# Kernel tuning notes

Measured on AMD Instinct MI355X. Metric: run time of the kernel, lower is better.

## Reference

```python
import jax, jax.numpy as jnp
import numpy as np

B, LQ, LK, D = 8, 1024, 4096, 1024


def setup_inputs() -> dict:
    key = jax.random.key(0)
    k1, k2, k3, k4, k5, k6 = jax.random.split(key, 6)
    s = 1.0 / np.sqrt(D)
    return {
        "T": jax.random.normal(k1, (B, LQ, D), dtype=jnp.float32),
        "S": jax.random.normal(k2, (B, LK, D), dtype=jnp.float32),
        "Wq": jax.random.uniform(k3, (D, D), jnp.float32, -s, s),
        "Wk": jax.random.uniform(k4, (D, D), jnp.float32, -s, s),
        "Wv": jax.random.uniform(k5, (D, D), jnp.float32, -s, s),
        "Wo": jax.random.uniform(k6, (D, D), jnp.float32, -s, s),
    }


def reference(T, S, Wq, Wk, Wv, Wo):
    # Linear layers: y = x @ W.T (torch nn.Linear convention), bias=False
    q = jnp.einsum('bqd,ed->bqe', T, Wq)          # [B, LQ, D]
    k = jnp.einsum('bkd,ed->bke', S, Wk)          # [B, LK, D]
    v = jnp.einsum('bkd,ed->bke', S, Wv)          # [B, LK, D]
    scale = jnp.asarray(D, q.dtype) ** -0.5        # hidden_dim ** -0.5 (single head)
    attn = jnp.einsum('bqe,bke->bqk', q, k) * scale  # [B, LQ, LK]
    attn = jax.nn.softmax(attn, axis=-1)
    out = jnp.einsum('bqk,bke->bqe', attn, v)      # [B, LQ, D]
    return jnp.einsum('bqe,fe->bqf', out, Wo)      # output projection
```

## Files before the change

kernel.cpp:

```cpp
#include <hip/hip_runtime.h>
#include <stdint.h>

typedef __bf16 bf16;
typedef __bf16 bf16x8 __attribute__((ext_vector_type(8)));
typedef float f32x4 __attribute__((ext_vector_type(4)));

__device__ __forceinline__ void gload_lds16(const void* g, void* l) {
    __builtin_amdgcn_global_load_lds(
        (const __attribute__((address_space(1))) unsigned int*)g,
        (__attribute__((address_space(3))) unsigned int*)l, 16, 0, 0);
}

#define BAR()    asm volatile("s_barrier" ::: "memory")
#define WAITV(N) asm volatile("s_waitcnt vmcnt(" #N ")" ::: "memory")

template<int OMODE>
__global__ __launch_bounds__(512, 2)
void gemm256(const bf16* __restrict__ A, const bf16* __restrict__ B,
             void* __restrict__ Cv, int K, int N,
             long batchA, long batchB, long batchC, float alpha,
             int nbx, int nby, int GC, int lda, int ldb)
{
    __shared__ __align__(16) bf16 lds[2][4][8192];

    const int nwg  = gridDim.x;
    const int orig = blockIdx.x;
    const int q8   = nwg >> 3, r8 = nwg & 7;
    const int xcd  = orig & 7, lid = orig >> 3;
    int p = (xcd < r8 ? xcd * (q8 + 1) : r8 * (q8 + 1) + (xcd - r8) * q8) + lid;

    int hv = 0;
    if constexpr (OMODE == 3) { hv = p >> 7; p &= 127; }
    const int kOff = hv << 11;

    const int perb = nbx * nby;
    const int z    = p / perb;
    const int pb   = p - z * perb;
    const int sw   = nby * GC;
    const int st   = pb / sw;
    const int rem  = pb - st * sw;
    const int by   = rem / GC;
    const int bx   = st * GC + (rem - by * GC);

    const long rowb = (long)by << 8;
    const long colb = (long)bx << 8;

    const int t  = threadIdx.x;
    const int l  = t & 63;
    const int w  = t >> 6;
    const int wm = w >> 2;
    const int wn = w & 3;

    const int sL   = (t * 16) ^ (((t >> 3) & 3) << 4);
    const int srow = sL >> 6;
    const int sk   = (sL & 63) >> 1;
    const bf16* gA = A + (long)z * batchA + (rowb + srow) * (long)lda + sk + kOff;
    const bf16* gB = B + (long)z * batchB + (colb + srow) * (long)ldb + sk + kOff;
    const long rA = 128L * lda;
    const long rB = 128L * ldb;
    const int  d0 = t * 8, d1 = t * 8 + 4096;

    const int xl    = ((l >> 1) & 3) << 4;
    const int aBase = ((wm * 128 + (l & 15)) * 64 + ((l >> 4) << 4)) ^ xl;
    const int bBase = ((wn * 64  + (l & 15)) * 64 + ((l >> 4) << 4)) ^ xl;

    f32x4 acc[8][4] = {};
    bf16x8 av[4], bv[4];

#define STG(S, R, G, KOFF2, RS) do { \
    const bf16* _g = (G) + (KOFF2); \
    gload_lds16(_g,      &lds[S][R][d0]); \
    gload_lds16(_g + RS, &lds[S][R][d1]); \
  } while (0)

#define RD(S, R, OFF) (*(const bf16x8*)((const char*)&lds[S][R][0] + (OFF)))

#define MM(MB) \
    __builtin_amdgcn_s_setprio(1); \
    _Pragma("unroll") for (int mi = 0; mi < 4; ++mi) \
      _Pragma("unroll") for (int nj = 0; nj < 4; ++nj) \
        acc[MB + mi][nj] = __builtin_amdgcn_mfma_f32_16x16x32_bf16(av[mi], bv[nj], acc[MB + mi][nj], 0, 0, 0); \
    __builtin_amdgcn_s_setprio(0);

#define PH1(S, STGX) { \
    _Pragma("unroll") for (int nj = 0; nj < 4; ++nj) bv[nj] = RD(S, 2, bBase + nj * 1024); \
    _Pragma("unroll") for (int mi = 0; mi < 4; ++mi) av[mi] = RD(S, 0, aBase + mi * 1024); \
    STGX; BAR(); MM(0) BAR(); }

#define PH2(S, STGX) { \
    _Pragma("unroll") for (int mi = 0; mi < 4; ++mi) av[mi] = RD(S, 0, aBase + 4096 + mi * 1024); \
    STGX; BAR(); MM(4) BAR(); }

#define PH3(S, STGX) { \
    _Pragma("unroll") for (int nj = 0; nj < 4; ++nj) bv[nj] = RD(S, 3, bBase + nj * 1024); \
    _Pragma("unroll") for (int mi = 0; mi < 4; ++mi) av[mi] = RD(S, 1, aBase + mi * 1024); \
    STGX; BAR(); MM(0) BAR(); }

#define PH4(S, STGX, WT) { \
    _Pragma("unroll") for (int mi = 0; mi < 4; ++mi) av[mi] = RD(S, 1, aBase + 4096 + mi * 1024); \
    STGX; BAR(); MM(4) WT; BAR(); }

    STG(0, 0, gA, 0,  rA);
    STG(0, 1, gA, 32, rA);
    STG(0, 2, gB, 0,  rB);
    STG(0, 3, gB, 32, rB);
    STG(1, 2, gB, 64, rB);
    STG(1, 0, gA, 64, rA);
    STG(1, 3, gB, 96, rB);
    WAITV(6);
    BAR();

    const int NI = K >> 7;
    for (int i = 0; i < NI - 1; ++i) {
        const int kb = i << 7;
        const int kn = kb + 128;
        PH1(0, STG(1, 1, gA, kb + 96, rA));
        PH2(0, STG(0, 2, gB, kn,      rB));
        PH3(0, STG(0, 0, gA, kn,      rA));
        PH4(0, STG(0, 3, gB, kn + 32, rB), WAITV(6));
        PH1(1, STG(0, 1, gA, kn + 32, rA));
        PH2(1, STG(1, 2, gB, kn + 64, rB));
        PH3(1, STG(1, 0, gA, kn + 64, rA));
        PH4(1, STG(1, 3, gB, kn + 96, rB), WAITV(6));
    }
    {
        const int kb = (NI - 1) << 7;
        PH1(0, STG(1, 1, gA, kb + 96, rA));
        PH2(0, );
        PH3(0, );
        PH4(0, , WAITV(0));
        PH1(1, );
        PH2(1, );
        PH3(1, );
        PH4(1, , );
    }
#undef STG
#undef RD
#undef MM
#undef PH1
#undef PH2
#undef PH3
#undef PH4

    const int r0 = (l >> 4) << 2;

    if constexpr (OMODE == 2) {
        const long cb0 = colb + wn * 64 + (l & 15);
        const long rb0 = rowb + wm * 128 + r0;
#pragma unroll
        for (int mf = 0; mf < 8; ++mf)
#pragma unroll
          for (int nj = 0; nj < 4; ++nj) {
            const long col = cb0 + nj * 16;
#pragma unroll
            for (int r = 0; r < 4; ++r) {
                const long row = rb0 + mf * 16 + r;
                ((float*)Cv)[(long)z * batchC + row * (long)N + col] = acc[mf][nj][r] * alpha;
            }
          }
    } else if constexpr (OMODE == 3) {
        float* Cb = (float*)Cv + (long)hv * 8388608 + (long)z * 1048576;
        const long cb0 = colb + wn * 64 + (l & 15);
        const long rb0 = rowb + wm * 128 + r0;
#pragma unroll
        for (int mf = 0; mf < 8; ++mf)
#pragma unroll
          for (int nj = 0; nj < 4; ++nj) {
            const long col = cb0 + nj * 16;
#pragma unroll
            for (int r = 0; r < 4; ++r)
                Cb[(rb0 + mf * 16 + r) * 1024 + col] = acc[mf][nj][r];
          }
    } else {
        bf16* epi = &lds[0][0][0];
        const int rrow   = t >> 5;
        const int cchunk = (t & 31) << 3;
        const int myh = (OMODE != 1) ? wm : (wn >> 1);
#pragma unroll
        for (int h = 0; h < 2; ++h) {
            if (myh == h) {
#pragma unroll
                for (int mf = 0; mf < 8; ++mf)
#pragma unroll
                  for (int nj = 0; nj < 4; ++nj)
#pragma unroll
                    for (int r = 0; r < 4; ++r) {
                        float v = acc[mf][nj][r] * alpha;
                        if constexpr (OMODE == 4) v = __expf(v);
                        int orow = wm * 128 + mf * 16 + r0 + r;
                        int ocol = wn * 64 + nj * 16 + (l & 15);
                        if (OMODE == 1) { int tmp = orow; orow = ocol; ocol = tmp; }
                        epi[(orow - h * 128) * 280 + ocol] = (bf16)v;
                    }
            }
            __syncthreads();
#pragma unroll
            for (int pp = 0; pp < 8; ++pp) {
                const int lrow = pp * 16 + rrow;
                const int row  = h * 128 + lrow;
                uint4 d = *(const uint4*)&epi[lrow * 280 + cchunk];
                if (OMODE != 1) {
                    bf16* Cb = (bf16*)Cv + (long)z * batchC;
                    *(uint4*)&Cb[(rowb + row) * (long)N + colb + cchunk] = d;
                } else {
                    const long zz  = rowb >> 12;
                    const long lk0 = (rowb & 4095) + cchunk;
                    *(uint4*)&((bf16*)Cv)[zz * 4194304L + (colb + row) * 4096L + lk0] = d;
                }
            }
            __syncthreads();
        }
    }
}

__global__ void cvt_bf16(const float* __restrict__ in, bf16* __restrict__ out, long n8)
{
    const long stride = (long)gridDim.x * 256;
    for (long i = (long)blockIdx.x * 256 + threadIdx.x; i < n8; i += stride) {
        const float4* p = (const float4*)in + i * 2;
        float4 a = p[0], b = p[1];
        union { bf16 h[8]; uint4 u; } o;
        o.h[0] = (bf16)a.x; o.h[1] = (bf16)a.y; o.h[2] = (bf16)a.z; o.h[3] = (bf16)a.w;
        o.h[4] = (bf16)b.x; o.h[5] = (bf16)b.y; o.h[6] = (bf16)b.z; o.h[7] = (bf16)b.w;
        ((uint4*)out)[i] = o.u;
    }
}

__global__ void cvt_w4(const float* __restrict__ wq, const float* __restrict__ wk,
                       const float* __restrict__ wv, const float* __restrict__ wo,
                       bf16* __restrict__ out)
{
    const long i  = (long)blockIdx.x * 256 + threadIdx.x;
    const int seg = (int)(i >> 17);
    const long j  = i & 131071;
    const float* src = seg == 0 ? wq : seg == 1 ? wk : seg == 2 ? wv : wo;
    const float4* pp = (const float4*)src + j * 2;
    float4 a = pp[0], b = pp[1];
    union { bf16 h[8]; uint4 u; } o;
    o.h[0] = (bf16)a.x; o.h[1] = (bf16)a.y; o.h[2] = (bf16)a.z; o.h[3] = (bf16)a.w;
    o.h[4] = (bf16)b.x; o.h[5] = (bf16)b.y; o.h[6] = (bf16)b.z; o.h[7] = (bf16)b.w;
    ((uint4*)out)[i] = o.u;
}

__global__ __launch_bounds__(256)
void rowsum(const bf16* __restrict__ P, float* __restrict__ sums)
{
    const long base = (long)blockIdx.x * 4096;
    const int t = threadIdx.x;
    union U { uint4 u; bf16 h[8]; };
    U d0, d1;
    d0.u = *(const uint4*)&P[base + t * 8];
    d1.u = *(const uint4*)&P[base + 2048 + t * 8];
    float s = 0.f;
#pragma unroll
    for (int i = 0; i < 8; ++i) s += (float)d0.h[i] + (float)d1.h[i];
    for (int o = 32; o; o >>= 1) s += __shfl_xor(s, o);
    __shared__ float reds[4];
    if ((t & 63) == 0) reds[t >> 6] = s;
    __syncthreads();
    if (t == 0) sums[blockIdx.x] = reds[0] + reds[1] + reds[2] + reds[3];
}

__global__ void reduce_pv(const float* __restrict__ Pt, const float* __restrict__ sums,
                          bf16* __restrict__ Ob)
{
    const long i = (long)blockIdx.x * 256 + threadIdx.x;
    const float inv = 1.f / sums[i >> 7];
    const float4* a = (const float4*)Pt + i * 2;
    const float4* b = (const float4*)(Pt + 8388608) + i * 2;
    float4 x0 = a[0], x1 = a[1], y0 = b[0], y1 = b[1];
    union { bf16 h[8]; uint4 u; } o;
    o.h[0] = (bf16)((x0.x + y0.x) * inv); o.h[1] = (bf16)((x0.y + y0.y) * inv);
    o.h[2] = (bf16)((x0.z + y0.z) * inv); o.h[3] = (bf16)((x0.w + y0.w) * inv);
    o.h[4] = (bf16)((x1.x + y1.x) * inv); o.h[5] = (bf16)((x1.y + y1.y) * inv);
    o.h[6] = (bf16)((x1.z + y1.z) * inv); o.h[7] = (bf16)((x1.w + y1.w) * inv);
    ((uint4*)Ob)[i] = o.u;
}

extern "C" void kernel_launch(void* const* d_in, const int* in_sizes, int n_in,
                              void* d_out, int out_size, void* d_ws, size_t ws_size,
                              hipStream_t stream)
{
    (void)in_sizes; (void)n_in; (void)out_size; (void)ws_size;
    const float* T  = (const float*)d_in[0];
    const float* S  = (const float*)d_in[1];
    const float* Wq = (const float*)d_in[2];
    const float* Wk = (const float*)d_in[3];
    const float* Wv = (const float*)d_in[4];
    const float* Wo = (const float*)d_in[5];
    float* Y = (float*)d_out;
    char* ws = (char*)d_ws;

    bf16* Wqb = (bf16*)(ws + 0);
    bf16* Wkb = (bf16*)(ws + 2097152);
    bf16* Wvb = (bf16*)(ws + 4194304);
    bf16* Wob = (bf16*)(ws + 6291456);
    bf16* Tb  = (bf16*)(ws + 8388608);
    bf16* Ob  = Tb;
    bf16* Qb  = (bf16*)(ws + 25165824);
    float* Sm = (float*)Qb;
    bf16* Sb  = (bf16*)(ws + 41943040);
    bf16* Pb  = Sb;
    bf16* Kb  = (bf16*)(ws + 109051904);
    float* Pt = (float*)Kb;
    bf16* VTb = (bf16*)(ws + 176160768);

    cvt_w4  <<<2048,  256, 0, stream>>>(Wq, Wk, Wv, Wo, Wqb);
    cvt_bf16<<<4096,  256, 0, stream>>>(T, Tb, 1048576);
    cvt_bf16<<<16384, 256, 0, stream>>>(S, Sb, 4194304);

    gemm256<0><<<128, 512, 0, stream>>>(Tb, Wqb, Qb, 1024, 1024,
        0, 0, 0, 1.f, 4, 32, 4, 1024, 1024);
    gemm256<0><<<512, 512, 0, stream>>>(Sb, Wkb, Kb, 1024, 1024,
        0, 0, 0, 1.f, 4, 128, 4, 1024, 1024);
    gemm256<1><<<512, 512, 0, stream>>>(Sb, Wvb, VTb, 1024, 1024,
        0, 0, 0, 1.f, 4, 128, 4, 1024, 1024);

    gemm256<4><<<512, 512, 0, stream>>>(Qb, Kb, Pb, 1024, 4096,
        1024L * 1024, 4096L * 1024, 1024L * 4096, 0.03125f, 16, 4, 4, 1024, 1024);

    rowsum<<<8192, 256, 0, stream>>>(Pb, Sm);

    gemm256<3><<<256, 512, 0, stream>>>(Pb, VTb, Pt, 2048, 1024,
        1024L * 4096, 1024L * 4096, 1048576, 1.f, 4, 4, 4, 4096, 4096);
    reduce_pv<<<4096, 256, 0, stream>>>(Pt, Sm, Ob);

    gemm256<2><<<128, 512, 0, stream>>>(Ob, Wob, Y, 1024, 1024,
        0, 0, 0, 1.f, 4, 32, 4, 1024, 1024);
}
```

Baseline: 415.0 us.

## Merge QKV projections into one launch and fuse softmax row sums into exp epilogue

The three Q/K/V projection GEMMs become a single 1152-block kernel that picks its operands and output from the block index, so the three launches and their tail imbalance collapse into one. The QK^T exp epilogue now computes partial row sums of each 256-column tile while it stores, and writes them to a small buffer. A tiny sum16 kernel then reduces the 16 partials per row, replacing the rowsum pass that re-read the whole bf16 probability matrix. The partial-sum buffers reuse workspace that held the Q/K weight copies, which are no longer needed by then. The cost is extra shuffles and stores inside the GEMM epilogue.

```diff
diff --git a/kernel.cpp b/kernel.cpp
--- a/kernel.cpp
+++ b/kernel.cpp
@@ -13,13 +13,163 @@
 
 #define BAR()    asm volatile("s_barrier" ::: "memory")
 #define WAITV(N) asm volatile("s_waitcnt vmcnt(" #N ")" ::: "memory")
+
+#define STG(S, R, G, KOFF2, RS) do { \
+    const bf16* _g = (G) + (KOFF2); \
+    gload_lds16(_g,      &lds[S][R][d0]); \
+    gload_lds16(_g + RS, &lds[S][R][d1]); \
+  } while (0)
+
+#define RD(S, R, OFF) (*(const bf16x8*)((const char*)&lds[S][R][0] + (OFF)))
+
+#define MM(MB) \
+    __builtin_amdgcn_s_setprio(1); \
+    _Pragma("unroll") for (int mi = 0; mi < 4; ++mi) \
+      _Pragma("unroll") for (int nj = 0; nj < 4; ++nj) \
+        acc[MB + mi][nj] = __builtin_amdgcn_mfma_f32_16x16x32_bf16(av[mi], bv[nj], acc[MB + mi][nj], 0, 0, 0); \
+    __builtin_amdgcn_s_setprio(0);
+
+#define PH1(S, STGX) { \
+    _Pragma("unroll") for (int nj = 0; nj < 4; ++nj) bv[nj] = RD(S, 2, bBase + nj * 1024); \
+    _Pragma("unroll") for (int mi = 0; mi < 4; ++mi) av[mi] = RD(S, 0, aBase + mi * 1024); \
+    STGX; BAR(); MM(0) BAR(); }
+
+#define PH2(S, STGX) { \
+    _Pragma("unroll") for (int mi = 0; mi < 4; ++mi) av[mi] = RD(S, 0, aBase + 4096 + mi * 1024); \
+    STGX; BAR(); MM(4) BAR(); }
+
+#define PH3(S, STGX) { \
+    _Pragma("unroll") for (int nj = 0; nj < 4; ++nj) bv[nj] = RD(S, 3, bBase + nj * 1024); \
+    _Pragma("unroll") for (int mi = 0; mi < 4; ++mi) av[mi] = RD(S, 1, aBase + mi * 1024); \
+    STGX; BAR(); MM(0) BAR(); }
+
+#define PH4(S, STGX, WT) { \
+    _Pragma("unroll") for (int mi = 0; mi < 4; ++mi) av[mi] = RD(S, 1, aBase + 4096 + mi * 1024); \
+    STGX; BAR(); MM(4) WT; BAR(); }
+
+__global__ __launch_bounds__(512, 2)
+void gemm_qkv(const bf16* __restrict__ Tb, const bf16* __restrict__ Sb,
+              const bf16* __restrict__ Wq, const bf16* __restrict__ Wk,
+              const bf16* __restrict__ Wv,
+              bf16* __restrict__ Qo, bf16* __restrict__ Ko, bf16* __restrict__ VTo)
+{
+    __shared__ __align__(16) bf16 lds[2][4][8192];
+
+    const int nwg  = gridDim.x;
+    const int orig = blockIdx.x;
+    const int q8   = nwg >> 3, r8 = nwg & 7;
+    const int xcd  = orig & 7, lid = orig >> 3;
+    const int p    = (xcd < r8 ? xcd * (q8 + 1) : r8 * (q8 + 1) + (xcd - r8) * q8) + lid;
+
+    const bf16 *A, *Bw; bf16 *Co; bool vt = false;
+    int lp;
+    if (p < 512)       { lp = p;        A = Sb; Bw = Wk; Co = Ko; }
+    else if (p < 1024) { lp = p - 512;  A = Sb; Bw = Wv; Co = VTo; vt = true; }
+    else               { lp = p - 1024; A = Tb; Bw = Wq; Co = Qo; }
+
+    const long rowb = (long)(lp >> 2) << 8;
+    const long colb = (long)(lp & 3) << 8;
+
+    const int t  = threadIdx.x;
+    const int l  = t & 63;
+    const int w  = t >> 6;
+    const int wm = w >> 2;
+    const int wn = w & 3;
+    const int l15 = l & 15;
+    const int r0  = (l >> 4) << 2;
+
+    const int sL   = (t * 16) ^ (((t >> 3) & 3) << 4);
+    const int srow = sL >> 6;
+    const int sk   = (sL & 63) >> 1;
+    const bf16* gA = A + (rowb + srow) * 1024 + sk;
+    const bf16* gB = Bw + (colb + srow) * 1024 + sk;
+    const long rA = 131072, rB = 131072;
+    const int  d0 = t * 8, d1 = t * 8 + 4096;
+
+    const int xl    = ((l >> 1) & 3) << 4;
+    const int aBase = ((wm * 128 + l15) * 64 + ((l >> 4) << 4)) ^ xl;
+    const int bBase = ((wn * 64  + l15) * 64 + ((l >> 4) << 4)) ^ xl;
+
+    f32x4 acc[8][4] = {};
+    bf16x8 av[4], bv[4];
+
+    STG(0, 0, gA, 0,  rA);
+    STG(0, 1, gA, 32, rA);
+    STG(0, 2, gB, 0,  rB);
+    STG(0, 3, gB, 32, rB);
+    STG(1, 2, gB, 64, rB);
+    STG(1, 0, gA, 64, rA);
+    STG(1, 3, gB, 96, rB);
+    WAITV(6);
+    BAR();
+
+    for (int i = 0; i < 7; ++i) {
+        const int kb = i << 7;
+        const int kn = kb + 128;
+        PH1(0, STG(1, 1, gA, kb + 96, rA));
+        PH2(0, STG(0, 2, gB, kn,      rB));
+        PH3(0, STG(0, 0, gA, kn,      rA));
+        PH4(0, STG(0, 3, gB, kn + 32, rB), WAITV(6));
+        PH1(1, STG(0, 1, gA, kn + 32, rA));
+        PH2(1, STG(1, 2, gB, kn + 64, rB));
+        PH3(1, STG(1, 0, gA, kn + 64, rA));
+        PH4(1, STG(1, 3, gB, kn + 96, rB), WAITV(6));
+    }
+    {
+        PH1(0, STG(1, 1, gA, 7 * 128 + 96, rA));
+        PH2(0, );
+        PH3(0, );
+        PH4(0, , WAITV(0));
+        PH1(1, );
+        PH2(1, );
+        PH3(1, );
+        PH4(1, , );
+    }
+
+    bf16* epi = &lds[0][0][0];
+    const int rrow   = t >> 5;
+    const int cchunk = (t & 31) << 3;
+    const int myh = vt ? (wn >> 1) : wm;
+#pragma unroll
+    for (int h = 0; h < 2; ++h) {
+        if (myh == h) {
+#pragma unroll
+            for (int mf = 0; mf < 8; ++mf)
+#pragma unroll
+              for (int nj = 0; nj < 4; ++nj)
+#pragma unroll
+                for (int r = 0; r < 4; ++r) {
+                    int orow = wm * 128 + mf * 16 + r0 + r;
+                    int ocol = wn * 64 + nj * 16 + l15;
+                    if (vt) { int tmp = orow; orow = ocol; ocol = tmp; }
+                    epi[(orow - h * 128) * 280 + ocol] = (bf16)acc[mf][nj][r];
+                }
+        }
+        __syncthreads();
+#pragma unroll
+        for (int pp = 0; pp < 8; ++pp) {
+            const int lrow = pp * 16 + rrow;
+            const int row  = h * 128 + lrow;
+            uint4 d = *(const uint4*)&epi[lrow * 280 + cchunk];
+            if (!vt) {
+                *(uint4*)&Co[(rowb + row) * 1024 + colb + cchunk] = d;
+            } else {
+                const long zz  = rowb >> 12;
+                const long lk0 = (rowb & 4095) + cchunk;
+                *(uint4*)&Co[zz * 4194304L + (colb + row) * 4096L + lk0] = d;
+            }
+        }
+        __syncthreads();
+    }
+}
 
 template<int OMODE>
 __global__ __launch_bounds__(512, 2)
 void gemm256(const bf16* __restrict__ A, const bf16* __restrict__ B,
              void* __restrict__ Cv, int K, int N,
              long batchA, long batchB, long batchC, float alpha,
-             int nbx, int nby, int GC, int lda, int ldb)
+             int nbx, int nby, int GC, int lda, int ldb,
+             float* __restrict__ Smp)
 {
     __shared__ __align__(16) bf16 lds[2][4][8192];
 
@@ -50,6 +200,8 @@
     const int w  = t >> 6;
     const int wm = w >> 2;
     const int wn = w & 3;
+    const int l15 = l & 15;
+    const int r0  = (l >> 4) << 2;
 
     const int sL   = (t * 16) ^ (((t >> 3) & 3) << 4);
     const int srow = sL >> 6;
@@ -61,44 +213,11 @@
     const int  d0 = t * 8, d1 = t * 8 + 4096;
 
     const int xl    = ((l >> 1) & 3) << 4;
-    const int aBase = ((wm * 128 + (l & 15)) * 64 + ((l >> 4) << 4)) ^ xl;
-    const int bBase = ((wn * 64  + (l & 15)) * 64 + ((l >> 4) << 4)) ^ xl;
+    const int aBase = ((wm * 128 + l15) * 64 + ((l >> 4) << 4)) ^ xl;
+    const int bBase = ((wn * 64  + l15) * 64 + ((l >> 4) << 4)) ^ xl;
 
     f32x4 acc[8][4] = {};
     bf16x8 av[4], bv[4];
-
-#define STG(S, R, G, KOFF2, RS) do { \
-    const bf16* _g = (G) + (KOFF2); \
-    gload_lds16(_g,      &lds[S][R][d0]); \
-    gload_lds16(_g + RS, &lds[S][R][d1]); \
-  } while (0)
-
-#define RD(S, R, OFF) (*(const bf16x8*)((const char*)&lds[S][R][0] + (OFF)))
-
-#define MM(MB) \
-    __builtin_amdgcn_s_setprio(1); \
-    _Pragma("unroll") for (int mi = 0; mi < 4; ++mi) \
-      _Pragma("unroll") for (int nj = 0; nj < 4; ++nj) \
-        acc[MB + mi][nj] = __builtin_amdgcn_mfma_f32_16x16x32_bf16(av[mi], bv[nj], acc[MB + mi][nj], 0, 0, 0); \
-    __builtin_amdgcn_s_setprio(0);
-
-#define PH1(S, STGX) { \
-    _Pragma("unroll") for (int nj = 0; nj < 4; ++nj) bv[nj] = RD(S, 2, bBase + nj * 1024); \
-    _Pragma("unroll") for (int mi = 0; mi < 4; ++mi) av[mi] = RD(S, 0, aBase + mi * 1024); \
-    STGX; BAR(); MM(0) BAR(); }
-
-#define PH2(S, STGX) { \
-    _Pragma("unroll") for (int mi = 0; mi < 4; ++mi) av[mi] = RD(S, 0, aBase + 4096 + mi * 1024); \
-    STGX; BAR(); MM(4) BAR(); }
-
-#define PH3(S, STGX) { \
-    _Pragma("unroll") for (int nj = 0; nj < 4; ++nj) bv[nj] = RD(S, 3, bBase + nj * 1024); \
-    _Pragma("unroll") for (int mi = 0; mi < 4; ++mi) av[mi] = RD(S, 1, aBase + mi * 1024); \
-    STGX; BAR(); MM(0) BAR(); }
-
-#define PH4(S, STGX, WT) { \
-    _Pragma("unroll") for (int mi = 0; mi < 4; ++mi) av[mi] = RD(S, 1, aBase + 4096 + mi * 1024); \
-    STGX; BAR(); MM(4) WT; BAR(); }
 
     STG(0, 0, gA, 0,  rA);
     STG(0, 1, gA, 32, rA);
@@ -134,6 +253,77 @@
         PH3(1, );
         PH4(1, , );
     }
+
+    if constexpr (OMODE == 2) {
+        const long cb0 = colb + wn * 64 + l15;
+        const long rb0 = rowb + wm * 128 + r0;
+#pragma unroll
+        for (int mf = 0; mf < 8; ++mf)
+#pragma unroll
+          for (int nj = 0; nj < 4; ++nj) {
+            const long col = cb0 + nj * 16;
+#pragma unroll
+            for (int r = 0; r < 4; ++r)
+                ((float*)Cv)[(long)z * batchC + (rb0 + mf * 16 + r) * (long)N + col]
+                    = acc[mf][nj][r] * alpha;
+          }
+    } else if constexpr (OMODE == 3) {
+        float* Cb = (float*)Cv + (long)hv * 8388608 + (long)z * 1048576;
+        const long cb0 = colb + wn * 64 + l15;
+        const long rb0 = rowb + wm * 128 + r0;
+#pragma unroll
+        for (int mf = 0; mf < 8; ++mf)
+#pragma unroll
+          for (int nj = 0; nj < 4; ++nj) {
+            const long col = cb0 + nj * 16;
+#pragma unroll
+            for (int r = 0; r < 4; ++r)
+                Cb[(rb0 + mf * 16 + r) * 1024 + col] = acc[mf][nj][r];
+          }
+    } else {
+        bf16* epi = &lds[0][0][0];
+        const int rrow   = t >> 5;
+        const int cchunk = (t & 31) << 3;
+#pragma unroll
+        for (int h = 0; h < 2; ++h) {
+            if (wm == h) {
+#pragma unroll
+                for (int mf = 0; mf < 8; ++mf)
+#pragma unroll
+                  for (int nj = 0; nj < 4; ++nj)
+#pragma unroll
+                    for (int r = 0; r < 4; ++r) {
+                        const float v = __expf(acc[mf][nj][r] * alpha);
+                        const int orow = wm * 128 + mf * 16 + r0 + r;
+                        const int ocol = wn * 64 + nj * 16 + l15;
+                        epi[(orow - h * 128) * 280 + ocol] = (bf16)v;
+                    }
+            }
+            __syncthreads();
+#pragma unroll
+            for (int pp = 0; pp < 8; ++pp) {
+                const int lrow = pp * 16 + rrow;
+                const int row  = h * 128 + lrow;
+                union { uint4 u; bf16 h8[8]; } ud;
+                ud.u = *(const uint4*)&epi[lrow * 280 + cchunk];
+                bf16* Cb = (bf16*)Cv + (long)z * batchC;
+                *(uint4*)&Cb[(rowb + row) * (long)N + colb + cchunk] = ud.u;
+                float s = 0.f;
+#pragma unroll
+                for (int j = 0; j < 8; ++j) s += (float)ud.h8[j];
+                s += __shfl_xor(s, 1);
+                s += __shfl_xor(s, 2);
+                s += __shfl_xor(s, 4);
+                s += __shfl_xor(s, 8);
+                s += __shfl_xor(s, 16);
+                if ((t & 31) == 0)
+                    Smp[((long)z * 1024 + rowb + row) * 16 + (colb >> 8)] = s;
+            }
+            __syncthreads();
+        }
+    }
+}
+
 #undef STG
 #undef RD
 #undef MM
@@ -141,77 +331,6 @@
 #undef PH2
 #undef PH3
 #undef PH4
-
-    const int r0 = (l >> 4) << 2;
-
-    if constexpr (OMODE == 2) {
-        const long cb0 = colb + wn * 64 + (l & 15);
-        const long rb0 = rowb + wm * 128 + r0;
-#pragma unroll
-        for (int mf = 0; mf < 8; ++mf)
-#pragma unroll
-          for (int nj = 0; nj < 4; ++nj) {
-            const long col = cb0 + nj * 16;
-#pragma unroll
-            for (int r = 0; r < 4; ++r) {
-                const long row = rb0 + mf * 16 + r;
-                ((float*)Cv)[(long)z * batchC + row * (long)N + col] = acc[mf][nj][r] * alpha;
-            }
-          }
-    } else if constexpr (OMODE == 3) {
-        float* Cb = (float*)Cv + (long)hv * 8388608 + (long)z * 1048576;
-        const long cb0 = colb + wn * 64 + (l & 15);
-        const long rb0 = rowb + wm * 128 + r0;
-#pragma unroll
-        for (int mf = 0; mf < 8; ++mf)
-#pragma unroll
-          for (int nj = 0; nj < 4; ++nj) {
-            const long col = cb0 + nj * 16;
-#pragma unroll
-            for (int r = 0; r < 4; ++r)
-                Cb[(rb0 + mf * 16 + r) * 1024 + col] = acc[mf][nj][r];
-          }
-    } else {
-        bf16* epi = &lds[0][0][0];
-        const int rrow   = t >> 5;
-        const int cchunk = (t & 31) << 3;
-        const int myh = (OMODE != 1) ? wm : (wn >> 1);
-#pragma unroll
-        for (int h = 0; h < 2; ++h) {
-            if (myh == h) {
-#pragma unroll
-                for (int mf = 0; mf < 8; ++mf)
-#pragma unroll
-                  for (int nj = 0; nj < 4; ++nj)
-#pragma unroll
-                    for (int r = 0; r < 4; ++r) {
-                        float v = acc[mf][nj][r] * alpha;
-                        if constexpr (OMODE == 4) v = __expf(v);
-                        int orow = wm * 128 + mf * 16 + r0 + r;
-                        int ocol = wn * 64 + nj * 16 + (l & 15);
-                        if (OMODE == 1) { int tmp = orow; orow = ocol; ocol = tmp; }
-                        epi[(orow - h * 128) * 280 + ocol] = (bf16)v;
-                    }
-            }
-            __syncthreads();
-#pragma unroll
-            for (int pp = 0; pp < 8; ++pp) {
-                const int lrow = pp * 16 + rrow;
-                const int row  = h * 128 + lrow;
-                uint4 d = *(const uint4*)&epi[lrow * 280 + cchunk];
-                if (OMODE != 1) {
-                    bf16* Cb = (bf16*)Cv + (long)z * batchC;
-                    *(uint4*)&Cb[(rowb + row) * (long)N + colb + cchunk] = d;
-                } else {
-                    const long zz  = rowb >> 12;
-                    const long lk0 = (rowb & 4095) + cchunk;
-                    *(uint4*)&((bf16*)Cv)[zz * 4194304L + (colb + row) * 4096L + lk0] = d;
-                }
-            }
-            __syncthreads();
-        }
-    }
-}
 
 __global__ void cvt_bf16(const float* __restrict__ in, bf16* __restrict__ out, long n8)
 {
@@ -243,22 +362,13 @@
 }
 
 __global__ __launch_bounds__(256)
-void rowsum(const bf16* __restrict__ P, float* __restrict__ sums)
-{
-    const long base = (long)blockIdx.x * 4096;
-    const int t = threadIdx.x;
-    union U { uint4 u; bf16 h[8]; };
-    U d0, d1;
-    d0.u = *(const uint4*)&P[base + t * 8];
-    d1.u = *(const uint4*)&P[base + 2048 + t * 8];
-    float s = 0.f;
-#pragma unroll
-    for (int i = 0; i < 8; ++i) s += (float)d0.h[i] + (float)d1.h[i];
-    for (int o = 32; o; o >>= 1) s += __shfl_xor(s, o);
-    __shared__ float reds[4];
-    if ((t & 63) == 0) reds[t >> 6] = s;
-    __syncthreads();
-    if (t == 0) sums[blockIdx.x] = reds[0] + reds[1] + reds[2] + reds[3];
+void sum16(const float* __restrict__ Smp, float* __restrict__ Sm)
+{
+    const int r = blockIdx.x * 256 + threadIdx.x;
+    const float4* p4 = (const float4*)(Smp + (long)r * 16);
+    float4 a = p4[0], b = p4[1], c = p4[2], d = p4[3];
+    Sm[r] = ((a.x + a.y) + (a.z + a.w)) + ((b.x + b.y) + (b.z + b.w))
+          + ((c.x + c.y) + (c.z + c.w)) + ((d.x + d.y) + (d.z + d.w));
 }
 
 __global__ void reduce_pv(const float* __restrict__ Pt, const float* __restrict__ sums,
@@ -298,33 +408,29 @@
     bf16* Tb  = (bf16*)(ws + 8388608);
     bf16* Ob  = Tb;
     bf16* Qb  = (bf16*)(ws + 25165824);
-    float* Sm = (float*)Qb;
     bf16* Sb  = (bf16*)(ws + 41943040);
     bf16* Pb  = Sb;
     bf16* Kb  = (bf16*)(ws + 109051904);
     float* Pt = (float*)Kb;
     bf16* VTb = (bf16*)(ws + 176160768);
+    float* Sm  = (float*)ws;
+    float* Smp = (float*)(ws + 2097152);
 
     cvt_w4  <<<2048,  256, 0, stream>>>(Wq, Wk, Wv, Wo, Wqb);
     cvt_bf16<<<4096,  256, 0, stream>>>(T, Tb, 1048576);
     cvt_bf16<<<16384, 256, 0, stream>>>(S, Sb, 4194304);
 
-    gemm256<0><<<128, 512, 0, stream>>>(Tb, Wqb, Qb, 1024, 1024,
-        0, 0, 0, 1.f, 4, 32, 4, 1024, 1024);
-    gemm256<0><<<512, 512, 0, stream>>>(Sb, Wkb, Kb, 1024, 1024,
-        0, 0, 0, 1.f, 4, 128, 4, 1024, 1024);
-    gemm256<1><<<512, 512, 0, stream>>>(Sb, Wvb, VTb, 1024, 1024,
-        0, 0, 0, 1.f, 4, 128, 4, 1024, 1024);
+    gemm_qkv<<<1152, 512, 0, stream>>>(Tb, Sb, Wqb, Wkb, Wvb, Qb, Kb, VTb);
 
     gemm256<4><<<512, 512, 0, stream>>>(Qb, Kb, Pb, 1024, 4096,
-        1024L * 1024, 4096L * 1024, 1024L * 4096, 0.03125f, 16, 4, 4, 1024, 1024);
-
-    rowsum<<<8192, 256, 0, stream>>>(Pb, Sm);
+        1024L * 1024, 4096L * 1024, 1024L * 4096, 0.03125f, 16, 4, 4, 1024, 1024, Smp);
+
+    sum16<<<32, 256, 0, stream>>>(Smp, Sm);
 
     gemm256<3><<<256, 512, 0, stream>>>(Pb, VTb, Pt, 2048, 1024,
-        1024L * 4096, 1024L * 4096, 1048576, 1.f, 4, 4, 4, 4096, 4096);
+        1024L * 4096, 1024L * 4096, 1048576, 1.f, 4, 4, 4, 4096, 4096, nullptr);
     reduce_pv<<<4096, 256, 0, stream>>>(Pt, Sm, Ob);
 
     gemm256<2><<<128, 512, 0, stream>>>(Ob, Wob, Y, 1024, 1024,
-        0, 0, 0, 1.f, 4, 32, 4, 1024, 1024);
-}
+        0, 0, 0, 1.f, 4, 32, 4, 1024, 1024, nullptr);
+}
```

Measured after the change: 411.2 us. About the same (-0.9%).
